# Kernel tuning notes

Measured on AMD Instinct MI355X. Metric: run time of the kernel, lower is better.

Reference implementation:

```python
import jax, jax.numpy as jnp
import numpy as np

OUT, IN = 8192, 8192
TOKENS = 32


def setup_inputs() -> dict:
    key = jax.random.key(0)
    k_in, k_w, k_zp, k_s, k_b = jax.random.split(key, 5)
    return {
        "input": jax.random.normal(k_in, (TOKENS, IN), dtype=jnp.float32),
        # int8 quantized weight stored as the compressed parameter
        "weight_packed": jax.random.randint(k_w, (OUT, IN), -128, 128, dtype=jnp.int32).astype(jnp.int8),
        # per-output-channel asymmetric zero point and scale
        "weight_zero_point": jax.random.randint(k_zp, (OUT, 1), -8, 8, dtype=jnp.int32).astype(jnp.int8),
        "weight_scale": (jax.random.uniform(k_s, (OUT, 1), dtype=jnp.float32) * 0.01 + 1e-4),
        "bias": jax.random.normal(k_b, (OUT,), dtype=jnp.float32),
    }


def reference(input, weight_packed, weight_zero_point, weight_scale, bias):
    # Compressor.decompress_module: dequantize int8 weight per output channel
    # w[o, i] = (q[o, i] - zp[o]) * scale[o]   -> fp32 [OUT, IN]
    w = (weight_packed.astype(jnp.int32) - weight_zero_point.astype(jnp.int32)).astype(jnp.float32) * weight_scale
    # F.linear(input, w, bias): [T, IN] @ [OUT, IN]^T + [OUT]
    return jnp.einsum("ti,oi->to", input, w) + bias
```

## Files before the change

kernel.cpp:

```cpp
#include <hip/hip_runtime.h>
#include <stdint.h>

#define TOKENS 32
#define IN_DIM 8192
#define OUT_DIM 8192
#define KSPLIT 8

typedef __bf16 bf16x8 __attribute__((ext_vector_type(8)));
typedef float f32x16 __attribute__((ext_vector_type(16)));

static __device__ __forceinline__ uint32_t pk_bf16_2(float f0, float f1) {
    return __builtin_amdgcn_perm(__float_as_uint(f1), __float_as_uint(f0), 0x07060302u);
}

__global__ __launch_bounds__(512) void gemm_kernel(
        const float* __restrict__ in,
        const int* __restrict__ w,
        const int* __restrict__ zp,
        const float* __restrict__ scale,
        const float* __restrict__ bias,
        float* __restrict__ out) {
    const int tid = threadIdx.x;
    const int wv   = tid >> 6;
    const int lane = tid & 63;
    const int lo   = lane & 31;
    const int hi   = lane >> 5;
    const int obase = blockIdx.x * 32;

    const int KC = IN_DIM / KSPLIT;
    const int k0 = wv * KC;

    const float* __restrict__ ap = in + (size_t)lo * IN_DIM + k0 + hi * 8;
    const int*   __restrict__ bp = w  + (size_t)(obase + lo) * IN_DIM + k0 + hi * 8;

    f32x16 acc;
#pragma unroll
    for (int i = 0; i < 16; ++i) acc[i] = 0.f;
    float rs = 0.f;

#pragma unroll 4
    for (int ks = 0; ks < KC; ks += 16) {
        float4 a0 = *reinterpret_cast<const float4*>(ap + ks);
        float4 a1 = *reinterpret_cast<const float4*>(ap + ks + 4);
        int4   b0 = *reinterpret_cast<const int4*>(bp + ks);
        int4   b1 = *reinterpret_cast<const int4*>(bp + ks + 4);

        rs += (a0.x + a0.y) + (a0.z + a0.w) + (a1.x + a1.y) + (a1.z + a1.w);

        union { uint32_t u[4]; bf16x8 v; } af, bfr;
        af.u[0] = pk_bf16_2(a0.x, a0.y);
        af.u[1] = pk_bf16_2(a0.z, a0.w);
        af.u[2] = pk_bf16_2(a1.x, a1.y);
        af.u[3] = pk_bf16_2(a1.z, a1.w);
        bfr.u[0] = pk_bf16_2((float)b0.x, (float)b0.y);
        bfr.u[1] = pk_bf16_2((float)b0.z, (float)b0.w);
        bfr.u[2] = pk_bf16_2((float)b1.x, (float)b1.y);
        bfr.u[3] = pk_bf16_2((float)b1.z, (float)b1.w);

        acc = __builtin_amdgcn_mfma_f32_32x32x16_bf16(af.v, bfr.v, acc, 0, 0, 0);
    }

    __shared__ float red[KSPLIT][TOKENS * 32];
    __shared__ float rsl[2 * KSPLIT][32];
#pragma unroll
    for (int r = 0; r < 16; ++r) {
        const int m = (r & 3) + 8 * (r >> 2) + 4 * hi;
        red[wv][m * 32 + lo] = acc[r];
    }
    rsl[wv * 2 + hi][lo] = rs;
    __syncthreads();

    for (int i = tid; i < TOKENS * 32; i += 512) {
        float s = 0.f;
#pragma unroll
        for (int wvi = 0; wvi < KSPLIT; ++wvi) s += red[wvi][i];
        const int m = i >> 5;
        const int n = i & 31;
        const int o = obase + n;
        float rsum = 0.f;
#pragma unroll
        for (int j = 0; j < 2 * KSPLIT; ++j) rsum += rsl[j][m];
        out[(size_t)m * OUT_DIM + o] = scale[o] * (s - (float)zp[o] * rsum) + bias[o];
    }
}

extern "C" void kernel_launch(void* const* d_in, const int* in_sizes, int n_in,
                              void* d_out, int out_size, void* d_ws, size_t ws_size,
                              hipStream_t stream) {
    const float* in    = (const float*)d_in[0];
    const int*   wq    = (const int*)d_in[1];
    const int*   zp    = (const int*)d_in[2];
    const float* scale = (const float*)d_in[3];
    const float* bias  = (const float*)d_in[4];
    float* out = (float*)d_out;

    gemm_kernel<<<OUT_DIM / 32, 512, 0, stream>>>(in, wq, zp, scale, bias, out);
}
```

Baseline: 403.3 us.

## Double-buffer weight tiles into LDS via async global_load_lds with fewer waves

Cuts each block from 8 waves to 2, each covering half of K. Weight rows are streamed into swizzled, double-buffered LDS tiles with direct global-to-LDS loads, and the activation registers are prefetched one chunk ahead, using explicit vmcnt waits to overlap loads with MFMA work. The row-sum now uses bf16-truncated activations, so the zero-point correction matches the bf16 MFMA inputs. The risks are lower occupancy, with fewer waves per CU to hide latency, and high register pressure from the 32 prefetched float4 activation values.

Result: faster. 369.0 us (-8.5%).

```diff
diff --git a/kernel.cpp b/kernel.cpp
--- a/kernel.cpp
+++ b/kernel.cpp
@@ -4,7 +4,10 @@
 #define TOKENS 32
 #define IN_DIM 8192
 #define OUT_DIM 8192
-#define KSPLIT 8
+#define NWAVE 2
+#define BK 128
+#define KRANGE (IN_DIM / NWAVE)
+#define NCHUNK (KRANGE / BK)
 
 typedef __bf16 bf16x8 __attribute__((ext_vector_type(8)));
 typedef float f32x16 __attribute__((ext_vector_type(16)));
@@ -12,74 +15,123 @@
 static __device__ __forceinline__ uint32_t pk_bf16_2(float f0, float f1) {
     return __builtin_amdgcn_perm(__float_as_uint(f1), __float_as_uint(f0), 0x07060302u);
 }
+static __device__ __forceinline__ float trunc_bf(float f) {
+    return __uint_as_float(__float_as_uint(f) & 0xffff0000u);
+}
 
-__global__ __launch_bounds__(512) void gemm_kernel(
+__global__ __launch_bounds__(128, 1) void gemm_kernel(
         const float* __restrict__ in,
         const int* __restrict__ w,
         const int* __restrict__ zp,
         const float* __restrict__ scale,
         const float* __restrict__ bias,
         float* __restrict__ out) {
-    const int tid = threadIdx.x;
-    const int wv   = tid >> 6;
-    const int lane = tid & 63;
-    const int lo   = lane & 31;
-    const int hi   = lane >> 5;
+    __shared__ int lds[NWAVE][2][32][BK];
+
+    const int tid   = threadIdx.x;
+    const int wv    = tid >> 6;
+    const int lane  = tid & 63;
+    const int lo    = lane & 31;
+    const int hi    = lane >> 5;
     const int obase = blockIdx.x * 32;
+    const int k0    = wv * KRANGE;
 
-    const int KC = IN_DIM / KSPLIT;
-    const int k0 = wv * KC;
+    const int l5 = lane & 31;
+    const int r0 = hi;
 
-    const float* __restrict__ ap = in + (size_t)lo * IN_DIM + k0 + hi * 8;
-    const int*   __restrict__ bp = w  + (size_t)(obase + lo) * IN_DIM + k0 + hi * 8;
+    auto stage = [&](int c, int b) {
+#pragma unroll
+        for (int p = 0; p < 16; ++p) {
+            const int r  = p * 2 + r0;
+            const int swr = (r & 7) << 2;
+            const int* g = w + (size_t)(obase + r) * IN_DIM + k0 + c * BK
+                             + ((l5 * 4) ^ swr);
+            __builtin_amdgcn_global_load_lds(
+                (const __attribute__((address_space(1))) void*)g,
+                (__attribute__((address_space(3))) void*)&lds[wv][b][p * 2][0],
+                16, 0, 0);
+        }
+    };
+
+    const float* ain = in + (size_t)lo * IN_DIM + k0 + hi * 8;
+    auto aload = [&](int c, float4 (&ab)[16]) {
+#pragma unroll
+        for (int j = 0; j < 16; ++j)
+            ab[j] = *reinterpret_cast<const float4*>(ain + c * BK + (j >> 1) * 16 + (j & 1) * 4);
+    };
 
     f32x16 acc;
 #pragma unroll
     for (int i = 0; i < 16; ++i) acc[i] = 0.f;
     float rs = 0.f;
 
-#pragma unroll 4
-    for (int ks = 0; ks < KC; ks += 16) {
-        float4 a0 = *reinterpret_cast<const float4*>(ap + ks);
-        float4 a1 = *reinterpret_cast<const float4*>(ap + ks + 4);
-        int4   b0 = *reinterpret_cast<const int4*>(bp + ks);
-        int4   b1 = *reinterpret_cast<const int4*>(bp + ks + 4);
+    const int sw = (lo & 7) << 2;
+    const int* lrow0 = &lds[wv][0][lo][0];
+    const int* lrow1 = &lds[wv][1][lo][0];
 
-        rs += (a0.x + a0.y) + (a0.z + a0.w) + (a1.x + a1.y) + (a1.z + a1.w);
+    auto compute = [&](const int* lrow, const float4 (&ab)[16]) {
+#pragma unroll
+        for (int s = 0; s < 8; ++s) {
+            const int d0 = s * 16 + hi * 8;
+            const float4 a0 = ab[2 * s];
+            const float4 a1 = ab[2 * s + 1];
+            int4 b0 = *reinterpret_cast<const int4*>(lrow + (d0 ^ sw));
+            int4 b1 = *reinterpret_cast<const int4*>(lrow + ((d0 + 4) ^ sw));
 
-        union { uint32_t u[4]; bf16x8 v; } af, bfr;
-        af.u[0] = pk_bf16_2(a0.x, a0.y);
-        af.u[1] = pk_bf16_2(a0.z, a0.w);
-        af.u[2] = pk_bf16_2(a1.x, a1.y);
-        af.u[3] = pk_bf16_2(a1.z, a1.w);
-        bfr.u[0] = pk_bf16_2((float)b0.x, (float)b0.y);
-        bfr.u[1] = pk_bf16_2((float)b0.z, (float)b0.w);
-        bfr.u[2] = pk_bf16_2((float)b1.x, (float)b1.y);
-        bfr.u[3] = pk_bf16_2((float)b1.z, (float)b1.w);
+            rs += trunc_bf(a0.x) + trunc_bf(a0.y) + trunc_bf(a0.z) + trunc_bf(a0.w)
+                + trunc_bf(a1.x) + trunc_bf(a1.y) + trunc_bf(a1.z) + trunc_bf(a1.w);
 
-        acc = __builtin_amdgcn_mfma_f32_32x32x16_bf16(af.v, bfr.v, acc, 0, 0, 0);
+            union { uint32_t u[4]; bf16x8 v; } af, bf_;
+            af.u[0] = pk_bf16_2(a0.x, a0.y);
+            af.u[1] = pk_bf16_2(a0.z, a0.w);
+            af.u[2] = pk_bf16_2(a1.x, a1.y);
+            af.u[3] = pk_bf16_2(a1.z, a1.w);
+            bf_.u[0] = pk_bf16_2((float)b0.x, (float)b0.y);
+            bf_.u[1] = pk_bf16_2((float)b0.z, (float)b0.w);
+            bf_.u[2] = pk_bf16_2((float)b1.x, (float)b1.y);
+            bf_.u[3] = pk_bf16_2((float)b1.z, (float)b1.w);
+
+            acc = __builtin_amdgcn_mfma_f32_32x32x16_bf16(af.v, bf_.v, acc, 0, 0, 0);
+        }
+    };
+
+    float4 ab0[16], ab1[16];
+
+    stage(0, 0);
+    aload(0, ab0);
+    for (int cc = 0; cc < NCHUNK; cc += 2) {
+        stage(cc + 1, 1);
+        aload(cc + 1, ab1);
+        asm volatile("s_waitcnt vmcnt(32)" ::: "memory");
+        compute(lrow0, ab0);
+
+        if (cc + 2 < NCHUNK) {
+            stage(cc + 2, 0);
+            aload(cc + 2, ab0);
+            asm volatile("s_waitcnt vmcnt(32)" ::: "memory");
+        } else {
+            asm volatile("s_waitcnt vmcnt(0)" ::: "memory");
+        }
+        compute(lrow1, ab1);
     }
 
-    __shared__ float red[KSPLIT][TOKENS * 32];
-    __shared__ float rsl[2 * KSPLIT][32];
+    rs += __shfl_down(rs, 32);
+    __syncthreads();
+    float* red = (float*)&lds[0][0][0][0];
+    float* rsl = red + NWAVE * TOKENS * 32;
 #pragma unroll
     for (int r = 0; r < 16; ++r) {
         const int m = (r & 3) + 8 * (r >> 2) + 4 * hi;
-        red[wv][m * 32 + lo] = acc[r];
+        red[wv * (TOKENS * 32) + m * 32 + lo] = acc[r];
     }
-    rsl[wv * 2 + hi][lo] = rs;
+    if (lane < 32) rsl[wv * 32 + lane] = rs;
     __syncthreads();
 
-    for (int i = tid; i < TOKENS * 32; i += 512) {
-        float s = 0.f;
-#pragma unroll
-        for (int wvi = 0; wvi < KSPLIT; ++wvi) s += red[wvi][i];
-        const int m = i >> 5;
-        const int n = i & 31;
-        const int o = obase + n;
-        float rsum = 0.f;
-#pragma unroll
-        for (int j = 0; j < 2 * KSPLIT; ++j) rsum += rsl[j][m];
+    for (int idx = tid; idx < TOKENS * 32; idx += 128) {
+        const int m = idx >> 5;
+        const int o = obase + (idx & 31);
+        float s    = red[idx] + red[TOKENS * 32 + idx];
+        float rsum = rsl[m] + rsl[32 + m];
         out[(size_t)m * OUT_DIM + o] = scale[o] * (s - (float)zp[o] * rsum) + bias[o];
     }
 }
@@ -94,5 +146,5 @@
     const float* bias  = (const float*)d_in[4];
     float* out = (float*)d_out;
 
-    gemm_kernel<<<OUT_DIM / 32, 512, 0, stream>>>(in, wq, zp, scale, bias, out);
+    gemm_kernel<<<OUT_DIM / 32, 128, 0, stream>>>(in, wq, zp, scale, bias, out);
 }
```
